# Performance work log

Hardware: AMD Instinct MI355X
Metric: run time of the kernel (lower is better)

Reference implementation:

```python
import jax, jax.numpy as jnp
import numpy as np

HEADS = 8
DIM_HEAD = 64
SCALE = DIM_HEAD ** -0.5


def setup_inputs() -> dict:
    key = jax.random.key(0)
    ks = jax.random.split(key, 6)
    B, N, D = 1, 4096, 640
    INNER = HEADS * DIM_HEAD  # 512
    s = lambda fan_in: 1.0 / np.sqrt(fan_in)
    return {
        "x": jax.random.normal(ks[0], (B, N, D), dtype=jnp.float32),
        "Wq": jax.random.normal(ks[1], (D, INNER), dtype=jnp.float32) * s(D),
        "Wk": jax.random.normal(ks[2], (D, INNER), dtype=jnp.float32) * s(D),
        "Wv": jax.random.normal(ks[3], (D, INNER), dtype=jnp.float32) * s(D),
        "Wo": jax.random.normal(ks[4], (INNER, D), dtype=jnp.float32) * s(INNER),
        "bo": jnp.zeros((D,), dtype=jnp.float32),
    }


def reference(x, Wq, Wk, Wv, Wo, bo):
    B, N, _ = x.shape
    h, d = HEADS, DIM_HEAD
    # self-attention: context = x
    q = (x @ Wq).reshape(B, N, h, d).transpose(0, 2, 1, 3)  # [B,h,N,d]
    k = (x @ Wk).reshape(B, N, h, d).transpose(0, 2, 1, 3)
    v = (x @ Wv).reshape(B, N, h, d).transpose(0, 2, 1, 3)
    sim = jnp.einsum('bhid,bhjd->bhij', q, k) * SCALE  # [B,h,N,N]
    attn = jax.nn.softmax(sim, axis=-1)
    out = jnp.einsum('bhij,bhjd->bhid', attn, v)  # [B,h,N,d]
    out = out.transpose(0, 2, 1, 3).reshape(B, N, h * d)  # [B,N,inner]
    return out @ Wo + bo  # dropout p=0.0 is identity
```

## Files before the change

kernel.cpp:

```cpp
#include <hip/hip_runtime.h>
#include <math.h>

#define NSEQ   4096
#define DMODEL 640
#define NHEAD  8
#define DHEAD  64
#define INNER  512
#define KVSPLIT 2

typedef _Float16 f16;
typedef _Float16 f16x8 __attribute__((ext_vector_type(8)));
typedef _Float16 f16x4 __attribute__((ext_vector_type(4)));
typedef float    f32x4 __attribute__((ext_vector_type(4)));

#define MFMA16(a, b, c) __builtin_amdgcn_mfma_f32_16x16x32_f16((a), (b), (c), 0, 0, 0)

#define QSCALE 0.18033688011112042f

__device__ __forceinline__ void gl16(const f16* g, f16* l) {
    __builtin_amdgcn_global_load_lds(
        (const __attribute__((address_space(1))) unsigned int*)g,
        (__attribute__((address_space(3))) unsigned int*)l, 16, 0, 0);
}

__global__ __launch_bounds__(256) void cvt_x(const float* __restrict__ x,
                                             f16* __restrict__ xh) {
    int i = (blockIdx.x * 256 + threadIdx.x) * 8;
    float4 a = *(const float4*)&x[i];
    float4 b = *(const float4*)&x[i + 4];
    f16x8 o = {(f16)a.x, (f16)a.y, (f16)a.z, (f16)a.w,
               (f16)b.x, (f16)b.y, (f16)b.z, (f16)b.w};
    *(f16x8*)&xh[i] = o;
}

__global__ __launch_bounds__(256) void transpose_cvtW(
    const float* __restrict__ Wq, const float* __restrict__ Wk,
    const float* __restrict__ Wv, const float* __restrict__ Wo,
    f16* __restrict__ WTq, f16* __restrict__ WTk, f16* __restrict__ WTv,
    f16* __restrict__ WoT) {
    __shared__ __align__(16) f16 T[64][72];
    const int bz = blockIdx.z;
    const float* src = bz == 0 ? Wq : bz == 1 ? Wk : bz == 2 ? Wv : Wo;
    f16* dst = bz == 0 ? WTq : bz == 1 ? WTk : bz == 2 ? WTv : WoT;
    const int R = (bz < 3) ? DMODEL : INNER;
    const int C = (bz < 3) ? INNER : DMODEL;
    const int c0 = blockIdx.x * 64, r0 = blockIdx.y * 64;
    if (c0 >= C || r0 >= R) return;
    const int t = threadIdx.x;
    {
        int r = t >> 2, cb = (t & 3) * 16;
#pragma unroll
        for (int i = 0; i < 16; i += 4) {
            float4 v = *(const float4*)&src[(size_t)(r0 + r) * C + c0 + cb + i];
            T[cb + i + 0][r] = (f16)v.x;
            T[cb + i + 1][r] = (f16)v.y;
            T[cb + i + 2][r] = (f16)v.z;
            T[cb + i + 3][r] = (f16)v.w;
        }
    }
    __syncthreads();
    {
        int c = t >> 2, rb = (t & 3) * 16;
        f16* d = dst + (size_t)(c0 + c) * R + r0 + rb;
        *(f16x8*)d = *(const f16x8*)&T[c][rb];
        *(f16x8*)(d + 8) = *(const f16x8*)&T[c][rb + 8];
    }
}

__global__ __launch_bounds__(256) void qkv_gemm16(
    const f16* __restrict__ xh,
    const f16* __restrict__ WTq, const f16* __restrict__ WTk,
    const f16* __restrict__ WTv,
    f16* __restrict__ q16, f16* __restrict__ k16, f16* __restrict__ vT16)
{
    __shared__ __align__(16) f16 S[12288];
    f16* Xs = S;
    f16* Ws = S + 8192;

    const int bx = blockIdx.x;
    const int by = blockIdx.y;
    const int bz = blockIdx.z;
    const f16* WT = (bz == 0) ? WTq : (bz == 1) ? WTk : WTv;

    const int tid = threadIdx.x;
    const int w = tid >> 6, lane = tid & 63;
    const int lr = lane & 15, lc = lane >> 4;
    const int srow8 = lane >> 3;
    const int le = 8 * ((lane & 7) ^ srow8);
    const int swz0 = 8 * (lc ^ (lr & 7));
    const int swz1 = 8 * ((lc + 4) ^ (lr & 7));
    const int m0 = by * 128, n0 = bx * 64;

    f32x4 acc[2][4] = {};

    for (int s = 0; s < DMODEL / 64; ++s) {
        const int k0 = s * 64;
#pragma unroll
        for (int c = 0; c < 4; ++c) {
            const int cc = 4 * w + c;
            gl16(xh + (size_t)(m0 + cc * 8 + srow8) * DMODEL + k0 + le,
                 &Xs[cc * 512]);
        }
#pragma unroll
        for (int c = 0; c < 2; ++c) {
            const int cc = 2 * w + c;
            gl16(WT + (size_t)(n0 + cc * 8 + srow8) * DMODEL + k0 + le,
                 &Ws[cc * 512]);
        }
        __syncthreads();
        f16x8 a0[2], a1[2];
#pragma unroll
        for (int g = 0; g < 2; ++g) {
            const int row = 32 * w + 16 * g + lr;
            a0[g] = *(const f16x8*)&Xs[row * 64 + swz0];
            a1[g] = *(const f16x8*)&Xs[row * 64 + swz1];
        }
#pragma unroll
        for (int nt = 0; nt < 4; ++nt) {
            f16x8 b0 = *(const f16x8*)&Ws[(nt * 16 + lr) * 64 + swz0];
            f16x8 b1 = *(const f16x8*)&Ws[(nt * 16 + lr) * 64 + swz1];
#pragma unroll
            for (int g = 0; g < 2; ++g)
                acc[g][nt] = MFMA16(a1[g], b1, MFMA16(a0[g], b0, acc[g][nt]));
        }
        __syncthreads();
    }

    const float sc = (bz == 0) ? QSCALE : 1.0f;
    if (bz < 2) {
#pragma unroll
        for (int g = 0; g < 2; ++g)
#pragma unroll
            for (int nt = 0; nt < 4; ++nt)
#pragma unroll
                for (int r = 0; r < 4; ++r)
                    S[(32 * w + 16 * g + 4 * lc + r) * 72 + nt * 16 + lr] =
                        (f16)(acc[g][nt][r] * sc);
        __syncthreads();
        f16* ob = ((bz == 0) ? q16 : k16) + (size_t)bx * NSEQ * DHEAD;
#pragma unroll
        for (int p = 0; p < 2; ++p) {
            const int rr = p * 64 + (tid >> 2), cb = (tid & 3) * 16;
            f16* dst = ob + (size_t)(m0 + rr) * DHEAD + cb;
            *(f16x8*)dst = *(const f16x8*)&S[rr * 72 + cb];
            *(f16x8*)(dst + 8) = *(const f16x8*)&S[rr * 72 + cb + 8];
        }
    } else {
#pragma unroll
        for (int g = 0; g < 2; ++g)
#pragma unroll
            for (int nt = 0; nt < 4; ++nt)
#pragma unroll
                for (int r = 0; r < 4; ++r)
                    S[(nt * 16 + lr) * 136 + 32 * w + 16 * g + 4 * lc + r] =
                        (f16)acc[g][nt][r];
        __syncthreads();
        const int rr = tid >> 2, cb = (tid & 3) * 32;
        f16* dst = vT16 + ((size_t)bx * DHEAD + rr) * NSEQ + m0 + cb;
        *(f16x8*)dst        = *(const f16x8*)&S[rr * 136 + cb];
        *(f16x8*)(dst + 8)  = *(const f16x8*)&S[rr * 136 + cb + 8];
        *(f16x8*)(dst + 16) = *(const f16x8*)&S[rr * 136 + cb + 16];
        *(f16x8*)(dst + 24) = *(const f16x8*)&S[rr * 136 + cb + 24];
    }
}

__global__ __launch_bounds__(256, 2) void attn_fwd(
    const f16* __restrict__ q16, const f16* __restrict__ k16,
    const f16* __restrict__ vT16, f16* __restrict__ Opart,
    float* __restrict__ Ml)
{
    __shared__ __align__(16) f16 KsB[2][4096];
    __shared__ __align__(16) f16 VtB[4][4096];
    __shared__ __align__(16) f16 Ps[8192];

    const int lin = blockIdx.x + 32 * blockIdx.y + 256 * blockIdx.z;
    const int h  = lin & 7;
    const int qb = (lin >> 3) & 31;
    const int sp = lin >> 8;

    const int tid = threadIdx.x;
    const int w = tid >> 6, lane = tid & 63;
    const int lr = lane & 15, lc = lane >> 4;
    const int srow8 = lane >> 3;
    const int le = 8 * ((lane & 7) ^ srow8);
    const int swz0 = 8 * (lc ^ (lr & 7));
    const int swz1 = 8 * ((lc + 4) ^ (lr & 7));

    const f16* kp = k16 + ((size_t)h * NSEQ + sp * (NSEQ / KVSPLIT)) * DHEAD;
    const f16* vp = vT16 + (size_t)h * DHEAD * NSEQ + sp * (NSEQ / KVSPLIT);

    f16x8 qf[2][2];
#pragma unroll
    for (int g = 0; g < 2; ++g) {
        const f16* qp = q16 +
            ((size_t)h * NSEQ + qb * 128 + 32 * w + 16 * g + lr) * DHEAD;
        qf[g][0] = *(const f16x8*)&qp[lc * 8];
        qf[g][1] = *(const f16x8*)&qp[32 + lc * 8];
    }

    float m_run[2] = {-INFINITY, -INFINITY}, l_run[2] = {0.f, 0.f};
    f32x4 o[2][4] = {};
    f32x4 sA[2][4], sB[2][4];
    const int NT = NSEQ / KVSPLIT / 64;

#define PREFETCH(J, KB, VB) {                                                 \
    _Pragma("unroll")                                                         \
    for (int c = 0; c < 2; ++c) {                                             \
        const int cc = 2 * w + c;                                             \
        gl16(kp + (size_t)((J) * 64 + cc * 8 + srow8) * DHEAD + le,           \
             &KsB[KB][cc * 512]);                                             \
        gl16(vp + (size_t)(cc * 8 + srow8) * NSEQ + (J) * 64 + le,            \
             &VtB[VB][cc * 512]);                                             \
    } }

#define QKT(KB, S) {                                                          \
    const f32x4 z4 = {0.f, 0.f, 0.f, 0.f};                                    \
    _Pragma("unroll")                                                         \
    for (int t = 0; t < 4; ++t) {                                             \
        f16x8 ka = *(const f16x8*)&KsB[KB][(t * 16 + lr) * 64 + swz0];        \
        f16x8 kb = *(const f16x8*)&KsB[KB][(t * 16 + lr) * 64 + swz1];        \
        _Pragma("unroll")                                                     \
        for (int g = 0; g < 2; ++g)                                           \
            S[g][t] = MFMA16(kb, qf[g][1], MFMA16(ka, qf[g][0], z4));         \
    } }

#define FINISH(VB, S) {                                                       \
    float pm[2];                                                              \
    _Pragma("unroll")                                                         \
    for (int g = 0; g < 2; ++g) {                                             \
        float mm = S[g][0][0];                                                \
        _Pragma("unroll")                                                     \
        for (int t = 0; t < 4; ++t)                                           \
            _Pragma("unroll")                                                 \
            for (int r = 0; r < 4; ++r) mm = fmaxf(mm, S[g][t][r]);           \
        mm = fmaxf(mm, __shfl_xor(mm, 16));                                   \
        mm = fmaxf(mm, __shfl_xor(mm, 32));                                   \
        pm[g] = mm;                                                           \
    }                                                                         \
    if (__any((pm[0] > m_run[0]) | (pm[1] > m_run[1]))) {                     \
        _Pragma("unroll")                                                     \
        for (int g = 0; g < 2; ++g) {                                         \
            const float mn = fmaxf(m_run[g], pm[g]);                          \
            const float al = __builtin_amdgcn_exp2f(m_run[g] - mn);           \
            m_run[g] = mn;                                                    \
            l_run[g] *= al;                                                   \
            _Pragma("unroll")                                                 \
            for (int dt = 0; dt < 4; ++dt) o[g][dt] *= al;                    \
        }                                                                     \
    }                                                                         \
    _Pragma("unroll")                                                         \
    for (int g = 0; g < 2; ++g) {                                             \
        float ps = 0.f;                                                       \
        _Pragma("unroll")                                                     \
        for (int t = 0; t < 4; ++t)                                           \
            _Pragma("unroll")                                                 \
            for (int r = 0; r < 4; ++r) {                                     \
                S[g][t][r] = __builtin_amdgcn_exp2f(S[g][t][r] - m_run[g]);   \
                ps += S[g][t][r];                                             \
            }                                                                 \
        ps += __shfl_xor(ps, 16);                                             \
        ps += __shfl_xor(ps, 32);                                             \
        l_run[g] += ps;                                                       \
    }                                                                         \
    _Pragma("unroll")                                                         \
    for (int g = 0; g < 2; ++g) {                                             \
        const int row = 32 * w + 16 * g + lr;                                 \
        _Pragma("unroll")                                                     \
        for (int t = 0; t < 4; ++t) {                                         \
            f16x4 pk = {(f16)S[g][t][0], (f16)S[g][t][1],                     \
                        (f16)S[g][t][2], (f16)S[g][t][3]};                    \
            const int col = (16 * t + 4 * lc) ^ ((lr & 7) << 3);              \
            *(f16x4*)&Ps[row * 64 + col] = pk;                                \
        }                                                                     \
    }                                                                         \
    {                                                                         \
        f16x8 pb[2][2];                                                       \
        _Pragma("unroll")                                                     \
        for (int g = 0; g < 2; ++g) {                                         \
            const int row = 32 * w + 16 * g + lr;                             \
            pb[g][0] = *(const f16x8*)&Ps[row * 64 + swz0];                   \
            pb[g][1] = *(const f16x8*)&Ps[row * 64 + swz1];                   \
        }                                                                     \
        _Pragma("unroll")                                                     \
        for (int dt = 0; dt < 4; ++dt) {                                      \
            f16x8 va0 = *(const f16x8*)&VtB[VB][(dt * 16 + lr) * 64 + swz0];  \
            f16x8 va1 = *(const f16x8*)&VtB[VB][(dt * 16 + lr) * 64 + swz1];  \
            _Pragma("unroll")                                                 \
            for (int g = 0; g < 2; ++g)                                       \
                o[g][dt] = MFMA16(va1, pb[g][1],                              \
                                  MFMA16(va0, pb[g][0], o[g][dt]));           \
        }                                                                     \
    } }

#define BODY(J, U, SCUR, SPRV) {                                              \
    if ((J) + 1 < NT) PREFETCH((J) + 1, ((U) + 1) & 1, ((U) + 1) & 3);        \
    QKT((U) & 1, SCUR);                                                       \
    if ((J) > 0) FINISH(((U) + 3) & 3, SPRV);                                 \
    __syncthreads();                                                          \
    }

    PREFETCH(0, 0, 0);
    __syncthreads();

    BODY(0, 0, sA, sB);
    BODY(1, 1, sB, sA);
    BODY(2, 2, sA, sB);
    BODY(3, 3, sB, sA);
    for (int m = 1; m < 8; ++m) {
        const int j = 4 * m;
        BODY(j, 0, sA, sB);
        BODY(j + 1, 1, sB, sA);
        BODY(j + 2, 2, sA, sB);
        BODY(j + 3, 3, sB, sA);
    }
    FINISH(3, sB);

#undef BODY
#undef FINISH
#undef QKT
#undef PREFETCH

#pragma unroll
    for (int g = 0; g < 2; ++g) {
        const float linv = 1.0f / l_run[g];
        const size_t qg = (size_t)qb * 128 + 32 * w + 16 * g + lr;
        f16* ob = Opart + (((size_t)(sp * 8 + h)) * NSEQ + qg) * DHEAD;
#pragma unroll
        for (int dt = 0; dt < 4; ++dt) {
            f16x4 ov = {(f16)(o[g][dt][0] * linv), (f16)(o[g][dt][1] * linv),
                        (f16)(o[g][dt][2] * linv), (f16)(o[g][dt][3] * linv)};
            *(f16x4*)&ob[dt * 16 + 4 * lc] = ov;
        }
        if (lc == 0) {
            float2 ml = make_float2(m_run[g], l_run[g]);
            *(float2*)&Ml[(((size_t)(sp * 8 + h)) * NSEQ + qg) * 2] = ml;
        }
    }
}

__global__ __launch_bounds__(256) void out_gemm16(
    const f16* __restrict__ Opart, const float* __restrict__ Ml,
    const f16* __restrict__ WoT,
    const float* __restrict__ bias, float* __restrict__ C)
{
    __shared__ __align__(16) f16 Xs[4096];
    __shared__ __align__(16) f16 Ws[4096];

    const int bx = blockIdx.x;
    const int by = blockIdx.y;
    const int tid = threadIdx.x;
    const int w = tid >> 6, lane = tid & 63;
    const int lr = lane & 15, lc = lane >> 4;
    const int srow8 = lane >> 3;
    const int j = lane & 7;
    const int le = 8 * (j ^ srow8);
    const int swz0 = 8 * (lc ^ (lr & 7));
    const int swz1 = 8 * ((lc + 4) ^ (lr & 7));
    const int m0 = by * 64, n0 = bx * 64;

    f32x4 acc[4] = {};

    for (int s8 = 0; s8 < 8; ++s8) {
        const int k0 = s8 * 64;
#pragma unroll
        for (int c = 0; c < 2; ++c) {
            const int cc = w * 2 + c;
            gl16(WoT + (size_t)(n0 + cc * 8 + srow8) * INNER + k0 + le,
                 &Ws[cc * 512]);
            const int row = cc * 8 + srow8;
            const size_t q = (size_t)m0 + row;
            f16x8 o0 = *(const f16x8*)&Opart[((size_t)s8 * NSEQ + q) * DHEAD + 8 * j];
            f16x8 o1 = *(const f16x8*)&Opart[((size_t)(8 + s8) * NSEQ + q) * DHEAD + 8 * j];
            float2 ml0 = *(const float2*)&Ml[((size_t)s8 * NSEQ + q) * 2];
            float2 ml1 = *(const float2*)&Ml[((size_t)(8 + s8) * NSEQ + q) * 2];
            const float mx = fmaxf(ml0.x, ml1.x);
            float w0 = ml0.y * __builtin_amdgcn_exp2f(ml0.x - mx);
            float w1 = ml1.y * __builtin_amdgcn_exp2f(ml1.x - mx);
            const float inv = 1.0f / (w0 + w1);
            w0 *= inv; w1 *= inv;
            f16x8 a8;
#pragma unroll
            for (int e = 0; e < 8; ++e)
                a8[e] = (f16)((float)o0[e] * w0 + (float)o1[e] * w1);
            *(f16x8*)&Xs[row * 64 + 8 * (j ^ (row & 7))] = a8;
        }
        __syncthreads();
        f16x8 a0 = *(const f16x8*)&Xs[(16 * w + lr) * 64 + swz0];
        f16x8 a1 = *(const f16x8*)&Xs[(16 * w + lr) * 64 + swz1];
#pragma unroll
        for (int nt = 0; nt < 4; ++nt) {
            f16x8 b0 = *(const f16x8*)&Ws[(nt * 16 + lr) * 64 + swz0];
            f16x8 b1 = *(const f16x8*)&Ws[(nt * 16 + lr) * 64 + swz1];
            acc[nt] = MFMA16(a1, b1, MFMA16(a0, b0, acc[nt]));
        }
        __syncthreads();
    }

#pragma unroll
    for (int nt = 0; nt < 4; ++nt) {
        const float b = bias[n0 + nt * 16 + lr];
#pragma unroll
        for (int r = 0; r < 4; ++r)
            C[(size_t)(m0 + 16 * w + lc * 4 + r) * DMODEL + n0 + nt * 16 + lr] =
                acc[nt][r] + b;
    }
}

extern "C" void kernel_launch(void* const* d_in, const int* in_sizes, int n_in,
                              void* d_out, int out_size, void* d_ws, size_t ws_size,
                              hipStream_t stream) {
    const float* x  = (const float*)d_in[0];
    const float* Wq = (const float*)d_in[1];
    const float* Wk = (const float*)d_in[2];
    const float* Wv = (const float*)d_in[3];
    const float* Wo = (const float*)d_in[4];
    const float* bo = (const float*)d_in[5];
    float* out = (float*)d_out;

    char* base = (char*)d_ws;
    f16*   Opart = (f16*)base;
    f16*   xh    = (f16*)base;
    f16*   WTq   = xh + (size_t)NSEQ * DMODEL;
    f16*   WTk   = WTq + (size_t)INNER * DMODEL;
    f16*   WTv   = WTk + (size_t)INNER * DMODEL;
    float* Ml    = (float*)(base + 8388608);
    f16*   WoT   = (f16*)(base + 8912896);
    f16*   q16   = (f16*)(base + 9568256);
    f16*   k16   = q16 + (size_t)NHEAD * NSEQ * DHEAD;
    f16*   vT16  = k16 + (size_t)NHEAD * NSEQ * DHEAD;

    cvt_x<<<NSEQ * DMODEL / (256 * 8), 256, 0, stream>>>(x, xh);
    transpose_cvtW<<<dim3(10, 10, 4), 256, 0, stream>>>(
        Wq, Wk, Wv, Wo, WTq, WTk, WTv, WoT);

    qkv_gemm16<<<dim3(NHEAD, NSEQ / 128, 3), 256, 0, stream>>>(
        xh, WTq, WTk, WTv, q16, k16, vT16);
    attn_fwd<<<dim3(NSEQ / 128, NHEAD, KVSPLIT), 256, 0, stream>>>(
        q16, k16, vT16, Opart, Ml);
    out_gemm16<<<dim3(DMODEL / 64, NSEQ / 64), 256, 0, stream>>>(
        Opart, Ml, WoT, bo, out);
}
```

Measured before the change: 164.1 us.

## Fuse x conversion into QKV GEMM and split split-KV combine into own kernel

Drops the separate fp32-to-fp16 kernel for x: the QKV GEMM now loads fp32 x straight from global memory, converts it in registers and writes swizzled fp16 into LDS. The split-KV combine that ran inside out_gemm16 (recomputed once per column block) moves to a standalone combine_o kernel that writes a merged fp16 attention output. out_gemm16 then streams it asynchronously with global_load_lds. This removes one launch and redundant combine work, but the QKV GEMM now re-reads and re-converts fp32 x in each of its 24 column blocks, adds a new launch, and loses the async LDS load for x.

```diff
diff --git a/kernel.cpp b/kernel.cpp
--- a/kernel.cpp
+++ b/kernel.cpp
@@ -21,16 +21,6 @@
     __builtin_amdgcn_global_load_lds(
         (const __attribute__((address_space(1))) unsigned int*)g,
         (__attribute__((address_space(3))) unsigned int*)l, 16, 0, 0);
-}
-
-__global__ __launch_bounds__(256) void cvt_x(const float* __restrict__ x,
-                                             f16* __restrict__ xh) {
-    int i = (blockIdx.x * 256 + threadIdx.x) * 8;
-    float4 a = *(const float4*)&x[i];
-    float4 b = *(const float4*)&x[i + 4];
-    f16x8 o = {(f16)a.x, (f16)a.y, (f16)a.z, (f16)a.w,
-               (f16)b.x, (f16)b.y, (f16)b.z, (f16)b.w};
-    *(f16x8*)&xh[i] = o;
 }
 
 __global__ __launch_bounds__(256) void transpose_cvtW(
@@ -68,7 +58,7 @@
 }
 
 __global__ __launch_bounds__(256) void qkv_gemm16(
-    const f16* __restrict__ xh,
+    const float* __restrict__ x,
     const f16* __restrict__ WTq, const f16* __restrict__ WTk,
     const f16* __restrict__ WTv,
     f16* __restrict__ q16, f16* __restrict__ k16, f16* __restrict__ vT16)
@@ -91,15 +81,26 @@
     const int swz1 = 8 * ((lc + 4) ^ (lr & 7));
     const int m0 = by * 128, n0 = bx * 64;
 
+    const int arow = tid >> 1;
+    const int ag   = (tid & 1) * 4;
+
     f32x4 acc[2][4] = {};
 
     for (int s = 0; s < DMODEL / 64; ++s) {
         const int k0 = s * 64;
-#pragma unroll
-        for (int c = 0; c < 4; ++c) {
-            const int cc = 4 * w + c;
-            gl16(xh + (size_t)(m0 + cc * 8 + srow8) * DMODEL + k0 + le,
-                 &Xs[cc * 512]);
+        {
+            const float* xs = x + (size_t)(m0 + arow) * DMODEL + k0 + ag * 8;
+            float4 xa[8];
+#pragma unroll
+            for (int i = 0; i < 8; ++i) xa[i] = *(const float4*)&xs[i * 4];
+#pragma unroll
+            for (int i = 0; i < 4; ++i) {
+                f16x8 v = {(f16)xa[2 * i].x, (f16)xa[2 * i].y,
+                           (f16)xa[2 * i].z, (f16)xa[2 * i].w,
+                           (f16)xa[2 * i + 1].x, (f16)xa[2 * i + 1].y,
+                           (f16)xa[2 * i + 1].z, (f16)xa[2 * i + 1].w};
+                *(f16x8*)&Xs[arow * 64 + 8 * ((ag + i) ^ (arow & 7))] = v;
+            }
         }
 #pragma unroll
         for (int c = 0; c < 2; ++c) {
@@ -338,9 +339,32 @@
     }
 }
 
+__global__ __launch_bounds__(256) void combine_o(
+    const f16* __restrict__ Opart, const float* __restrict__ Ml,
+    f16* __restrict__ aoh)
+{
+    const int idx = (blockIdx.x * 256 + threadIdx.x) * 8;
+    const int q = idx >> 9;
+    const int c = idx & 511;
+    const int h = c >> 6, d = c & 63;
+    f16x8 o0 = *(const f16x8*)&Opart[((size_t)h * NSEQ + q) * DHEAD + d];
+    f16x8 o1 = *(const f16x8*)&Opart[((size_t)(8 + h) * NSEQ + q) * DHEAD + d];
+    float2 ml0 = *(const float2*)&Ml[((size_t)h * NSEQ + q) * 2];
+    float2 ml1 = *(const float2*)&Ml[((size_t)(8 + h) * NSEQ + q) * 2];
+    const float mx = fmaxf(ml0.x, ml1.x);
+    float w0 = ml0.y * __builtin_amdgcn_exp2f(ml0.x - mx);
+    float w1 = ml1.y * __builtin_amdgcn_exp2f(ml1.x - mx);
+    const float inv = 1.0f / (w0 + w1);
+    w0 *= inv; w1 *= inv;
+    f16x8 a8;
+#pragma unroll
+    for (int e = 0; e < 8; ++e)
+        a8[e] = (f16)((float)o0[e] * w0 + (float)o1[e] * w1);
+    *(f16x8*)&aoh[idx] = a8;
+}
+
 __global__ __launch_bounds__(256) void out_gemm16(
-    const f16* __restrict__ Opart, const float* __restrict__ Ml,
-    const f16* __restrict__ WoT,
+    const f16* __restrict__ aoh, const f16* __restrict__ WoT,
     const float* __restrict__ bias, float* __restrict__ C)
 {
     __shared__ __align__(16) f16 Xs[4096];
@@ -352,8 +376,7 @@
     const int w = tid >> 6, lane = tid & 63;
     const int lr = lane & 15, lc = lane >> 4;
     const int srow8 = lane >> 3;
-    const int j = lane & 7;
-    const int le = 8 * (j ^ srow8);
+    const int le = 8 * ((lane & 7) ^ srow8);
     const int swz0 = 8 * (lc ^ (lr & 7));
     const int swz1 = 8 * ((lc + 4) ^ (lr & 7));
     const int m0 = by * 64, n0 = bx * 64;
@@ -365,24 +388,10 @@
 #pragma unroll
         for (int c = 0; c < 2; ++c) {
             const int cc = w * 2 + c;
+            gl16(aoh + (size_t)(m0 + cc * 8 + srow8) * INNER + k0 + le,
+                 &Xs[cc * 512]);
             gl16(WoT + (size_t)(n0 + cc * 8 + srow8) * INNER + k0 + le,
                  &Ws[cc * 512]);
-            const int row = cc * 8 + srow8;
-            const size_t q = (size_t)m0 + row;
-            f16x8 o0 = *(const f16x8*)&Opart[((size_t)s8 * NSEQ + q) * DHEAD + 8 * j];
-            f16x8 o1 = *(const f16x8*)&Opart[((size_t)(8 + s8) * NSEQ + q) * DHEAD + 8 * j];
-            float2 ml0 = *(const float2*)&Ml[((size_t)s8 * NSEQ + q) * 2];
-            float2 ml1 = *(const float2*)&Ml[((size_t)(8 + s8) * NSEQ + q) * 2];
-            const float mx = fmaxf(ml0.x, ml1.x);
-            float w0 = ml0.y * __builtin_amdgcn_exp2f(ml0.x - mx);
-            float w1 = ml1.y * __builtin_amdgcn_exp2f(ml1.x - mx);
-            const float inv = 1.0f / (w0 + w1);
-            w0 *= inv; w1 *= inv;
-            f16x8 a8;
-#pragma unroll
-            for (int e = 0; e < 8; ++e)
-                a8[e] = (f16)((float)o0[e] * w0 + (float)o1[e] * w1);
-            *(f16x8*)&Xs[row * 64 + 8 * (j ^ (row & 7))] = a8;
         }
         __syncthreads();
         f16x8 a0 = *(const f16x8*)&Xs[(16 * w + lr) * 64 + swz0];
@@ -419,8 +428,7 @@
 
     char* base = (char*)d_ws;
     f16*   Opart = (f16*)base;
-    f16*   xh    = (f16*)base;
-    f16*   WTq   = xh + (size_t)NSEQ * DMODEL;
+    f16*   WTq   = (f16*)base;
     f16*   WTk   = WTq + (size_t)INNER * DMODEL;
     f16*   WTv   = WTk + (size_t)INNER * DMODEL;
     float* Ml    = (float*)(base + 8388608);
@@ -428,15 +436,16 @@
     f16*   q16   = (f16*)(base + 9568256);
     f16*   k16   = q16 + (size_t)NHEAD * NSEQ * DHEAD;
     f16*   vT16  = k16 + (size_t)NHEAD * NSEQ * DHEAD;
-
-    cvt_x<<<NSEQ * DMODEL / (256 * 8), 256, 0, stream>>>(x, xh);
+    f16*   aoh   = (f16*)(base + 22151168);
+
     transpose_cvtW<<<dim3(10, 10, 4), 256, 0, stream>>>(
         Wq, Wk, Wv, Wo, WTq, WTk, WTv, WoT);
 
     qkv_gemm16<<<dim3(NHEAD, NSEQ / 128, 3), 256, 0, stream>>>(
-        xh, WTq, WTk, WTv, q16, k16, vT16);
+        x, WTq, WTk, WTv, q16, k16, vT16);
     attn_fwd<<<dim3(NSEQ / 128, NHEAD, KVSPLIT), 256, 0, stream>>>(
         q16, k16, vT16, Opart, Ml);
+    combine_o<<<NSEQ * INNER / (256 * 8), 256, 0, stream>>>(Opart, Ml, aoh);
     out_gemm16<<<dim3(DMODEL / 64, NSEQ / 64), 256, 0, stream>>>(
-        Opart, Ml, WoT, bo, out);
-}
+        aoh, WoT, bo, out);
+}
```

After: 180.6 us. 10.1% more time.
